# Performance work log

Hardware: AMD Instinct MI355X
Metric: run time of the kernel (lower is better)

The kernel has to match this reference:

```python
import jax, jax.numpy as jnp
import numpy as np

NUM_EXPERTS = 8
D_IN = 4096
D_OUT = 4096


def setup_inputs() -> dict:
    key = jax.random.key(0)
    k_x, k_gw, k_gb, k_ew, k_eb = jax.random.split(key, 5)
    x = jax.random.normal(k_x, (4, 2048, D_IN), dtype=jnp.float32)
    gate_w = jax.random.normal(k_gw, (NUM_EXPERTS, D_IN), dtype=jnp.float32) * 0.02
    gate_b = jax.random.normal(k_gb, (NUM_EXPERTS,), dtype=jnp.float32) * 0.02
    expert_w = jax.random.normal(k_ew, (NUM_EXPERTS, D_OUT, D_IN), dtype=jnp.float32) * 0.02
    expert_b = jax.random.normal(k_eb, (NUM_EXPERTS, D_OUT), dtype=jnp.float32) * 0.02
    return {"x": x, "gate_w": gate_w, "gate_b": gate_b,
            "expert_w": expert_w, "expert_b": expert_b}


def reference(x, gate_w, gate_b, expert_w, expert_b):
    # Flatten tokens: [T, D_IN]
    orig_shape = x.shape
    xf = x.reshape(-1, x.shape[-1])
    # Gating: softmax over logits, then top-1 (argmax of softmax == argmax of logits)
    gate_logits = xf @ gate_w.T + gate_b            # [T, E]
    gates = jax.nn.softmax(gate_logits, axis=-1)
    selected = jnp.argmax(gates, axis=-1)           # [T] int
    # Per-expert Linear applied to the tokens routed to it (dense-masked grouped GEMM).
    # Faithful to the module: top-1 dispatch, no gate-probability weighting of output.
    out = jnp.zeros((xf.shape[0], expert_w.shape[1]), dtype=xf.dtype)
    for j in range(expert_w.shape[0]):  # fixed small expert count
        yj = xf @ expert_w[j].T + expert_b[j]       # [T, D_OUT]
        out = out + jnp.where((selected == j)[:, None], yj, 0.0)
    return out.reshape(*orig_shape[:-1], expert_w.shape[1])
```

## Files before the change

### kernel.cpp

```cpp
#include <hip/hip_runtime.h>

#define NE   8
#define DIN  4096
#define DOUT 4096
#define TOK  8192

#define BM 128
#define BN 128
#define BKF 64

#define BK 32
#define LDSK 40

typedef __attribute__((ext_vector_type(4))) float f32x4;
typedef __attribute__((ext_vector_type(8))) short bf16x8;
typedef __attribute__((ext_vector_type(2))) unsigned long long u64x2;

#define AS1 __attribute__((address_space(1)))
#define AS3 __attribute__((address_space(3)))

static __device__ __forceinline__ unsigned short f2bf(float f) {
  unsigned u = __builtin_bit_cast(unsigned, f);
  u += 0x7fffu + ((u >> 16) & 1u);
  return (unsigned short)(u >> 16);
}

static __device__ __forceinline__ unsigned long long pack4(f32x4 v) {
  return (unsigned long long)f2bf(v[0])
       | ((unsigned long long)f2bf(v[1]) << 16)
       | ((unsigned long long)f2bf(v[2]) << 32)
       | ((unsigned long long)f2bf(v[3]) << 48);
}

static __device__ __forceinline__ void gload16(const void* g, void* l) {
  __builtin_amdgcn_global_load_lds((const AS1 unsigned int*)g,
                                   (AS3 unsigned int*)l, 16, 0, 0);
}

__global__ void gate_convert(const float* __restrict__ x, const float* __restrict__ gw,
                             const float* __restrict__ gb, int* __restrict__ counts,
                             int* __restrict__ tlist, unsigned short* __restrict__ xbf) {
  const int lane = threadIdx.x & 63;
  const int tok  = blockIdx.x * 4 + (threadIdx.x >> 6);
  const float* xr = x + (size_t)tok * DIN;
  unsigned short* xo = xbf + (size_t)tok * DIN;
  float acc[NE];
  #pragma unroll
  for (int e = 0; e < NE; ++e) acc[e] = 0.f;
  for (int i = lane * 4; i < DIN; i += 256) {
    f32x4 xv = *(const f32x4*)(xr + i);
    *(unsigned long long*)(xo + i) = pack4(xv);
    #pragma unroll
    for (int e = 0; e < NE; ++e) {
      f32x4 wv = *(const f32x4*)(gw + e * DIN + i);
      acc[e] += xv[0]*wv[0] + xv[1]*wv[1] + xv[2]*wv[2] + xv[3]*wv[3];
    }
  }
  #pragma unroll
  for (int e = 0; e < NE; ++e) {
    float v = acc[e];
    #pragma unroll
    for (int o = 32; o > 0; o >>= 1) v += __shfl_xor(v, o);
    acc[e] = v;
  }
  if (lane == 0) {
    float bv = acc[0] + gb[0];
    int best = 0;
    #pragma unroll
    for (int e = 1; e < NE; ++e) {
      float v = acc[e] + gb[e];
      if (v > bv) { bv = v; best = e; }
    }
    int pos = atomicAdd(&counts[best], 1);
    tlist[best * TOK + pos] = tok;
  }
}

__global__ void convw(const float* __restrict__ w, unsigned short* __restrict__ wbf) {
  const size_t n = (size_t)NE * DOUT * DIN;
  size_t idx = ((size_t)blockIdx.x * 256 + threadIdx.x) * 8;
  const size_t stride = (size_t)gridDim.x * 256 * 8;
  for (; idx < n; idx += stride) {
    f32x4 a = *(const f32x4*)(w + idx);
    f32x4 b = *(const f32x4*)(w + idx + 4);
    u64x2 v; v[0] = pack4(a); v[1] = pack4(b);
    *(u64x2*)(wbf + idx) = v;
  }
}

__global__ __launch_bounds__(256, 2)
void moe_gemm_bf(const unsigned short* __restrict__ xbf,
                 const unsigned short* __restrict__ wbf,
                 const float* __restrict__ eb,
                 const int* __restrict__ counts,
                 const int* __restrict__ tlist,
                 float* __restrict__ out) {
  __shared__ unsigned short sA[BM * BKF];
  __shared__ unsigned short sB[BN * BKF];
  __shared__ int rowtok[BM];

  const int tid  = threadIdx.x;
  const int slot = blockIdx.y;

  int e = -1, mtile = 0, Me = 0;
  {
    int acc = 0;
    #pragma unroll
    for (int j = 0; j < NE; ++j) {
      int c = counts[j];
      int t = (c + BM - 1) / BM;
      if (e < 0 && slot < acc + t) { e = j; mtile = slot - acc; Me = c; }
      acc += t;
    }
  }
  if (e < 0) return;

  const int n0 = blockIdx.x * BN;
  const int m0 = mtile * BM;

  if (tid < BM) {
    int r = m0 + tid;
    rowtok[tid] = tlist[e * TOK + (r < Me ? r : Me - 1)];
  }
  __syncthreads();

  const int lane = tid & 63;
  const int w    = tid >> 6;
  const int j8   = lane & 7;
  const int rsub = lane >> 3;
  const int colsw = ((j8 ^ rsub) * 8);

  const unsigned short* ag[4];
  const unsigned short* bg[4];
  const unsigned short* wbase = wbf + (size_t)e * DOUT * DIN;
  #pragma unroll
  for (int c = 0; c < 4; ++c) {
    int row = (w * 4 + c) * 8 + rsub;
    ag[c] = xbf   + (size_t)rowtok[row] * DIN + colsw;
    bg[c] = wbase + (size_t)(n0 + row)  * DIN + colsw;
  }

  const int wr = (w >> 1) * 64;
  const int wc = (w & 1) * 64;
  const int lr = lane & 15;
  const int lk = lane >> 4;
  const int lr7 = lr & 7;

  f32x4 acc[4][4];
  #pragma unroll
  for (int m = 0; m < 4; ++m)
    #pragma unroll
    for (int n = 0; n < 4; ++n) acc[m][n] = (f32x4){0.f, 0.f, 0.f, 0.f};

  for (int kt = 0; kt < DIN / BKF; ++kt) {
    const int kofs = kt * BKF;
    #pragma unroll
    for (int c = 0; c < 4; ++c) {
      gload16(ag[c] + kofs, &sA[(w * 4 + c) * 512]);
      gload16(bg[c] + kofs, &sB[(w * 4 + c) * 512]);
    }
    __syncthreads();

    #pragma unroll
    for (int ks = 0; ks < 2; ++ks) {
      bf16x8 af[4], bfv[4];
      #pragma unroll
      for (int m = 0; m < 4; ++m)
        af[m] = *(const bf16x8*)&sA[(wr + m * 16 + lr) * BKF + (((ks * 4 + lk) ^ lr7) * 8)];
      #pragma unroll
      for (int n = 0; n < 4; ++n)
        bfv[n] = *(const bf16x8*)&sB[(wc + n * 16 + lr) * BKF + (((ks * 4 + lk) ^ lr7) * 8)];
      #pragma unroll
      for (int m = 0; m < 4; ++m)
        #pragma unroll
        for (int n = 0; n < 4; ++n)
          acc[m][n] = __builtin_amdgcn_mfma_f32_16x16x32_bf16(af[m], bfv[n], acc[m][n], 0, 0, 0);
    }
    __syncthreads();
  }

  float bias[4];
  #pragma unroll
  for (int n = 0; n < 4; ++n) bias[n] = eb[e * DOUT + n0 + wc + n * 16 + lr];

  #pragma unroll
  for (int m = 0; m < 4; ++m) {
    #pragma unroll
    for (int j = 0; j < 4; ++j) {
      int rloc = wr + m * 16 + lk * 4 + j;
      if (m0 + rloc < Me) {
        int tokr = rowtok[rloc];
        float* op = out + (size_t)tokr * DOUT + n0 + wc;
        #pragma unroll
        for (int n = 0; n < 4; ++n)
          op[n * 16 + lr] = acc[m][n][j] + bias[n];
      }
    }
  }
}

__global__ void gate_kernel(const float* __restrict__ x, const float* __restrict__ gw,
                            const float* __restrict__ gb, int* __restrict__ counts,
                            int* __restrict__ tlist) {
  const int lane = threadIdx.x & 63;
  const int tok  = blockIdx.x * 4 + (threadIdx.x >> 6);
  const float* xr = x + (size_t)tok * DIN;
  float acc[NE];
  #pragma unroll
  for (int e = 0; e < NE; ++e) acc[e] = 0.f;
  for (int i = lane; i < DIN; i += 64) {
    float xv = xr[i];
    #pragma unroll
    for (int e = 0; e < NE; ++e) acc[e] += xv * gw[e * DIN + i];
  }
  #pragma unroll
  for (int e = 0; e < NE; ++e) {
    float v = acc[e];
    #pragma unroll
    for (int o = 32; o > 0; o >>= 1) v += __shfl_xor(v, o);
    acc[e] = v;
  }
  if (lane == 0) {
    float bv = acc[0] + gb[0];
    int best = 0;
    #pragma unroll
    for (int e = 1; e < NE; ++e) {
      float v = acc[e] + gb[e];
      if (v > bv) { bv = v; best = e; }
    }
    int pos = atomicAdd(&counts[best], 1);
    tlist[best * TOK + pos] = tok;
  }
}

__global__ __launch_bounds__(256, 2)
void moe_gemm(const float* __restrict__ x, const float* __restrict__ ew,
              const float* __restrict__ eb, const int* __restrict__ counts,
              const int* __restrict__ tlist, float* __restrict__ out) {
  __shared__ unsigned short sA[2][BM * LDSK];
  __shared__ unsigned short sB[2][BN * LDSK];
  __shared__ int rowtok[BM];

  const int tid  = threadIdx.x;
  const int slot = blockIdx.y;

  int e = -1, mtile = 0, Me = 0;
  {
    int acc = 0;
    #pragma unroll
    for (int j = 0; j < NE; ++j) {
      int c = counts[j];
      int t = (c + BM - 1) / BM;
      if (e < 0 && slot < acc + t) { e = j; mtile = slot - acc; Me = c; }
      acc += t;
    }
  }
  if (e < 0) return;

  const int n0 = blockIdx.x * BN;
  const int m0 = mtile * BM;
  const float* we = ew + (size_t)e * DOUT * DIN;

  if (tid < BM) {
    int r = m0 + tid;
    int rr = r < Me ? r : (Me - 1);
    rowtok[tid] = tlist[e * TOK + rr];
  }
  __syncthreads();

  const int srow = tid >> 3;
  const int scol = (tid & 7) * 4;
  const int lane = tid & 63;
  const int w  = tid >> 6;
  const int wr = (w >> 1) * 64;
  const int wc = (w & 1) * 64;
  const int lr = lane & 15;
  const int lk = lane >> 4;

  f32x4 accf[4][4];
  #pragma unroll
  for (int m = 0; m < 4; ++m)
    #pragma unroll
    for (int n = 0; n < 4; ++n) accf[m][n] = (f32x4){0.f, 0.f, 0.f, 0.f};

  const float* aptr[4];
  const float* bptr[4];
  #pragma unroll
  for (int p = 0; p < 4; ++p) {
    int r = p * 32 + srow;
    aptr[p] = x  + (size_t)rowtok[r] * DIN + scol;
    bptr[p] = we + (size_t)(n0 + r)  * DIN + scol;
  }

  const int NK = DIN / BK;

  #pragma unroll
  for (int p = 0; p < 4; ++p) {
    int r = p * 32 + srow;
    *(unsigned long long*)&sA[0][r * LDSK + scol] = pack4(*(const f32x4*)(aptr[p]));
    *(unsigned long long*)&sB[0][r * LDSK + scol] = pack4(*(const f32x4*)(bptr[p]));
  }
  __syncthreads();

  int cur = 0;
  for (int kt = 0; kt < NK; ++kt) {
    f32x4 ra[4], rb[4];
    const bool more = (kt + 1 < NK);
    if (more) {
      const int koff = (kt + 1) * BK;
      #pragma unroll
      for (int p = 0; p < 4; ++p) {
        ra[p] = *(const f32x4*)(aptr[p] + koff);
        rb[p] = *(const f32x4*)(bptr[p] + koff);
      }
    }
    bf16x8 af[4], bfr[4];
    #pragma unroll
    for (int m = 0; m < 4; ++m)
      af[m] = *(const bf16x8*)&sA[cur][(wr + m * 16 + lr) * LDSK + lk * 8];
    #pragma unroll
    for (int n = 0; n < 4; ++n)
      bfr[n] = *(const bf16x8*)&sB[cur][(wc + n * 16 + lr) * LDSK + lk * 8];
    #pragma unroll
    for (int m = 0; m < 4; ++m)
      #pragma unroll
      for (int n = 0; n < 4; ++n)
        accf[m][n] = __builtin_amdgcn_mfma_f32_16x16x32_bf16(af[m], bfr[n], accf[m][n], 0, 0, 0);
    if (more) {
      #pragma unroll
      for (int p = 0; p < 4; ++p) {
        int r = p * 32 + srow;
        *(unsigned long long*)&sA[cur ^ 1][r * LDSK + scol] = pack4(ra[p]);
        *(unsigned long long*)&sB[cur ^ 1][r * LDSK + scol] = pack4(rb[p]);
      }
    }
    __syncthreads();
    cur ^= 1;
  }

  float bias[4];
  #pragma unroll
  for (int n = 0; n < 4; ++n) bias[n] = eb[e * DOUT + n0 + wc + n * 16 + lr];

  #pragma unroll
  for (int m = 0; m < 4; ++m) {
    #pragma unroll
    for (int j = 0; j < 4; ++j) {
      int rloc = wr + m * 16 + lk * 4 + j;
      if (m0 + rloc < Me) {
        int tokr = rowtok[rloc];
        float* op = out + (size_t)tokr * DOUT + n0 + wc;
        #pragma unroll
        for (int n = 0; n < 4; ++n)
          op[n * 16 + lr] = accf[m][n][j] + bias[n];
      }
    }
  }
}

extern "C" void kernel_launch(void* const* d_in, const int* in_sizes, int n_in,
                              void* d_out, int out_size, void* d_ws, size_t ws_size,
                              hipStream_t stream) {
  const float* x  = (const float*)d_in[0];
  const float* gw = (const float*)d_in[1];
  const float* gb = (const float*)d_in[2];
  const float* ew = (const float*)d_in[3];
  const float* eb = (const float*)d_in[4];
  float* out = (float*)d_out;

  int* counts = (int*)d_ws;
  int* tlist  = counts + 16;
  const size_t XOFF = 1u << 20;
  const size_t WOFF = XOFF + (size_t)TOK * DIN * 2;
  const size_t NEED = WOFF + (size_t)NE * DOUT * DIN * 2;

  hipMemsetAsync(counts, 0, 16 * sizeof(int), stream);

  if (ws_size >= NEED) {
    unsigned short* xbf = (unsigned short*)((char*)d_ws + XOFF);
    unsigned short* wbf = (unsigned short*)((char*)d_ws + WOFF);
    gate_convert<<<TOK / 4, 256, 0, stream>>>(x, gw, gb, counts, tlist, xbf);
    convw<<<8192, 256, 0, stream>>>(ew, wbf);
    dim3 grid(DOUT / BN, TOK / BM + NE, 1);
    moe_gemm_bf<<<grid, 256, 0, stream>>>(xbf, wbf, eb, counts, tlist, out);
  } else {
    gate_kernel<<<TOK / 4, 256, 0, stream>>>(x, gw, gb, counts, tlist);
    dim3 grid(DOUT / BN, TOK / BM + NE, 1);
    moe_gemm<<<grid, 256, 0, stream>>>(x, ew, eb, counts, tlist, out);
  }
}
```

Before: 606.5 us.

## Use 256x256 tiles, 512 threads, triple-buffered LDS pipeline and XCD-aware block remap

Rewrites the bf16 grouped GEMM to use 256x256 output tiles with 8 waves, each wave holding a 128x64 accumulator slice. LDS becomes a 3-stage ring of BK=32 tiles filled by direct global-to-LDS loads, with vmcnt-based waits and one barrier per step instead of two. The launch becomes a 1D grid whose block IDs are remapped so consecutive tiles share an XCD, and s_setprio is raised around MFMA bursts. The larger tiles give more reuse per byte loaded but raise register pressure and can waste work on partially filled expert tiles.

```diff
diff --git a/kernel.cpp b/kernel.cpp
--- a/kernel.cpp
+++ b/kernel.cpp
@@ -5,11 +5,14 @@
 #define DOUT 4096
 #define TOK  8192
 
-#define BM 128
-#define BN 128
-#define BKF 64
-
+#define BM 256
+#define BN 256
 #define BK 32
+#define NT (DIN / BK)
+#define TSZ (BM * BK)
+
+#define FBM 128
+#define FBK 32
 #define LDSK 40
 
 typedef __attribute__((ext_vector_type(4))) float f32x4;
@@ -30,11 +33,6 @@
        | ((unsigned long long)f2bf(v[1]) << 16)
        | ((unsigned long long)f2bf(v[2]) << 32)
        | ((unsigned long long)f2bf(v[3]) << 48);
-}
-
-static __device__ __forceinline__ void gload16(const void* g, void* l) {
-  __builtin_amdgcn_global_load_lds((const AS1 unsigned int*)g,
-                                   (AS3 unsigned int*)l, 16, 0, 0);
 }
 
 __global__ void gate_convert(const float* __restrict__ x, const float* __restrict__ gw,
@@ -88,19 +86,23 @@
   }
 }
 
-__global__ __launch_bounds__(256, 2)
+__global__ __launch_bounds__(512, 2)
 void moe_gemm_bf(const unsigned short* __restrict__ xbf,
                  const unsigned short* __restrict__ wbf,
                  const float* __restrict__ eb,
                  const int* __restrict__ counts,
                  const int* __restrict__ tlist,
                  float* __restrict__ out) {
-  __shared__ unsigned short sA[BM * BKF];
-  __shared__ unsigned short sB[BN * BKF];
+  __shared__ unsigned short sA[3 * TSZ];
+  __shared__ unsigned short sB[3 * TSZ];
   __shared__ int rowtok[BM];
 
-  const int tid  = threadIdx.x;
-  const int slot = blockIdx.y;
+  const int tid = threadIdx.x;
+
+  const int cpx  = gridDim.x >> 3;
+  const int wgid = (blockIdx.x & 7) * cpx + (blockIdx.x >> 3);
+  const int ntile = wgid & 15;
+  const int slot  = wgid >> 4;
 
   int e = -1, mtile = 0, Me = 0;
   {
@@ -115,8 +117,9 @@
   }
   if (e < 0) return;
 
-  const int n0 = blockIdx.x * BN;
+  const int n0 = ntile * BN;
   const int m0 = mtile * BM;
+  const unsigned short* wbase = wbf + (size_t)e * DOUT * DIN;
 
   if (tid < BM) {
     int r = m0 + tid;
@@ -124,79 +127,117 @@
   }
   __syncthreads();
 
-  const int lane = tid & 63;
-  const int w    = tid >> 6;
-  const int j8   = lane & 7;
-  const int rsub = lane >> 3;
-  const int colsw = ((j8 ^ rsub) * 8);
-
-  const unsigned short* ag[4];
-  const unsigned short* bg[4];
-  const unsigned short* wbase = wbf + (size_t)e * DOUT * DIN;
-  #pragma unroll
-  for (int c = 0; c < 4; ++c) {
-    int row = (w * 4 + c) * 8 + rsub;
-    ag[c] = xbf   + (size_t)rowtok[row] * DIN + colsw;
-    bg[c] = wbase + (size_t)(n0 + row)  * DIN + colsw;
-  }
-
-  const int wr = (w >> 1) * 64;
-  const int wc = (w & 1) * 64;
-  const int lr = lane & 15;
-  const int lk = lane >> 4;
-  const int lr7 = lr & 7;
-
-  f32x4 acc[4][4];
-  #pragma unroll
-  for (int m = 0; m < 4; ++m)
+  const int w = tid >> 6;
+  const int l = tid & 63;
+
+  const int sr0 = w * 32 + (l >> 2);
+  const int sr1 = sr0 + 16;
+  const int c0 = ((l & 3) ^ ((sr0 >> 1) & 3)) * 8;
+  const int c1 = ((l & 3) ^ ((sr1 >> 1) & 3)) * 8;
+  const unsigned short* ga0 = xbf   + (size_t)rowtok[sr0] * DIN + c0;
+  const unsigned short* ga1 = xbf   + (size_t)rowtok[sr1] * DIN + c1;
+  const unsigned short* gb0 = wbase + (size_t)(n0 + sr0)  * DIN + c0;
+  const unsigned short* gb1 = wbase + (size_t)(n0 + sr1)  * DIN + c1;
+  const int la0 = (w * 32) * BK;
+  const int la1 = (w * 32 + 16) * BK;
+
+  const int wm = w >> 2, wn = w & 3;
+  const int lr = l & 15, lk = l >> 4;
+  int offA[8], offB[4];
+  #pragma unroll
+  for (int m = 0; m < 8; ++m) {
+    int r = wm * 128 + m * 16 + lr;
+    offA[m] = r * BK + ((lk ^ ((r >> 1) & 3)) * 8);
+  }
+  #pragma unroll
+  for (int n = 0; n < 4; ++n) {
+    int r = wn * 64 + n * 16 + lr;
+    offB[n] = r * BK + ((lk ^ ((r >> 1) & 3)) * 8);
+  }
+
+  f32x4 acc[8][4];
+  #pragma unroll
+  for (int m = 0; m < 8; ++m)
     #pragma unroll
     for (int n = 0; n < 4; ++n) acc[m][n] = (f32x4){0.f, 0.f, 0.f, 0.f};
 
-  for (int kt = 0; kt < DIN / BKF; ++kt) {
-    const int kofs = kt * BKF;
-    #pragma unroll
-    for (int c = 0; c < 4; ++c) {
-      gload16(ag[c] + kofs, &sA[(w * 4 + c) * 512]);
-      gload16(bg[c] + kofs, &sB[(w * 4 + c) * 512]);
-    }
-    __syncthreads();
-
-    #pragma unroll
-    for (int ks = 0; ks < 2; ++ks) {
-      bf16x8 af[4], bfv[4];
-      #pragma unroll
-      for (int m = 0; m < 4; ++m)
-        af[m] = *(const bf16x8*)&sA[(wr + m * 16 + lr) * BKF + (((ks * 4 + lk) ^ lr7) * 8)];
-      #pragma unroll
-      for (int n = 0; n < 4; ++n)
-        bfv[n] = *(const bf16x8*)&sB[(wc + n * 16 + lr) * BKF + (((ks * 4 + lk) ^ lr7) * 8)];
-      #pragma unroll
-      for (int m = 0; m < 4; ++m)
-        #pragma unroll
-        for (int n = 0; n < 4; ++n)
-          acc[m][n] = __builtin_amdgcn_mfma_f32_16x16x32_bf16(af[m], bfv[n], acc[m][n], 0, 0, 0);
-    }
-    __syncthreads();
-  }
+#define STAGE(kt, b) do {                                                                   \
+    const int ko_ = (kt) * BK;                                                              \
+    const int bo_ = (b) * TSZ;                                                              \
+    __builtin_amdgcn_global_load_lds((const AS1 unsigned int*)(ga0 + ko_),                  \
+                                     (AS3 unsigned int*)&sA[bo_ + la0], 16, 0, 0);          \
+    __builtin_amdgcn_global_load_lds((const AS1 unsigned int*)(ga1 + ko_),                  \
+                                     (AS3 unsigned int*)&sA[bo_ + la1], 16, 0, 0);          \
+    __builtin_amdgcn_global_load_lds((const AS1 unsigned int*)(gb0 + ko_),                  \
+                                     (AS3 unsigned int*)&sB[bo_ + la0], 16, 0, 0);          \
+    __builtin_amdgcn_global_load_lds((const AS1 unsigned int*)(gb1 + ko_),                  \
+                                     (AS3 unsigned int*)&sB[bo_ + la1], 16, 0, 0);          \
+  } while (0)
+
+#define COMPUTE(b) do {                                                                     \
+    const int bo_ = (b) * TSZ;                                                              \
+    bf16x8 bv[4], av[4];                                                                    \
+    _Pragma("unroll") for (int n = 0; n < 4; ++n)                                           \
+      bv[n] = *(const bf16x8*)&sB[bo_ + offB[n]];                                           \
+    _Pragma("unroll") for (int m = 0; m < 4; ++m)                                           \
+      av[m] = *(const bf16x8*)&sA[bo_ + offA[m]];                                           \
+    __builtin_amdgcn_s_setprio(1);                                                          \
+    _Pragma("unroll") for (int m = 0; m < 4; ++m)                                           \
+      _Pragma("unroll") for (int n = 0; n < 4; ++n)                                         \
+        acc[m][n] = __builtin_amdgcn_mfma_f32_16x16x32_bf16(av[m], bv[n], acc[m][n], 0,0,0);\
+    __builtin_amdgcn_s_setprio(0);                                                          \
+    _Pragma("unroll") for (int m = 0; m < 4; ++m)                                           \
+      av[m] = *(const bf16x8*)&sA[bo_ + offA[m + 4]];                                       \
+    __builtin_amdgcn_s_setprio(1);                                                          \
+    _Pragma("unroll") for (int m = 0; m < 4; ++m)                                           \
+      _Pragma("unroll") for (int n = 0; n < 4; ++n)                                         \
+        acc[m+4][n] = __builtin_amdgcn_mfma_f32_16x16x32_bf16(av[m], bv[n], acc[m+4][n], 0,0,0);\
+    __builtin_amdgcn_s_setprio(0);                                                          \
+  } while (0)
+
+  STAGE(0, 0);
+  STAGE(1, 1);
+  asm volatile("s_waitcnt vmcnt(4)" ::: "memory");
+  __builtin_amdgcn_s_barrier();
+  asm volatile("" ::: "memory");
+
+  int ct = 0;
+  for (int t = 0; t < NT - 2; ++t) {
+    int bn = ct + 2; if (bn >= 3) bn -= 3;
+    STAGE(t + 2, bn);
+    COMPUTE(ct);
+    asm volatile("s_waitcnt vmcnt(4)" ::: "memory");
+    __builtin_amdgcn_s_barrier();
+    asm volatile("" ::: "memory");
+    ct = (ct == 2) ? 0 : ct + 1;
+  }
+  COMPUTE(ct);
+  asm volatile("s_waitcnt vmcnt(0)" ::: "memory");
+  __builtin_amdgcn_s_barrier();
+  asm volatile("" ::: "memory");
+  ct = (ct == 2) ? 0 : ct + 1;
+  COMPUTE(ct);
 
   float bias[4];
   #pragma unroll
-  for (int n = 0; n < 4; ++n) bias[n] = eb[e * DOUT + n0 + wc + n * 16 + lr];
-
-  #pragma unroll
-  for (int m = 0; m < 4; ++m) {
+  for (int n = 0; n < 4; ++n) bias[n] = eb[e * DOUT + n0 + wn * 64 + n * 16 + lr];
+
+  #pragma unroll
+  for (int m = 0; m < 8; ++m) {
     #pragma unroll
     for (int j = 0; j < 4; ++j) {
-      int rloc = wr + m * 16 + lk * 4 + j;
+      int rloc = wm * 128 + m * 16 + lk * 4 + j;
       if (m0 + rloc < Me) {
         int tokr = rowtok[rloc];
-        float* op = out + (size_t)tokr * DOUT + n0 + wc;
+        float* op = out + (size_t)tokr * DOUT + n0 + wn * 64;
         #pragma unroll
         for (int n = 0; n < 4; ++n)
           op[n * 16 + lr] = acc[m][n][j] + bias[n];
       }
     }
   }
+#undef STAGE
+#undef COMPUTE
 }
 
 __global__ void gate_kernel(const float* __restrict__ x, const float* __restrict__ gw,
@@ -237,9 +278,9 @@
 void moe_gemm(const float* __restrict__ x, const float* __restrict__ ew,
               const float* __restrict__ eb, const int* __restrict__ counts,
               const int* __restrict__ tlist, float* __restrict__ out) {
-  __shared__ unsigned short sA[2][BM * LDSK];
-  __shared__ unsigned short sB[2][BN * LDSK];
-  __shared__ int rowtok[BM];
+  __shared__ unsigned short fA[2][FBM * LDSK];
+  __shared__ unsigned short fB[2][FBM * LDSK];
+  __shared__ int rowtok[FBM];
 
   const int tid  = threadIdx.x;
   const int slot = blockIdx.y;
@@ -250,21 +291,20 @@
     #pragma unroll
     for (int j = 0; j < NE; ++j) {
       int c = counts[j];
-      int t = (c + BM - 1) / BM;
+      int t = (c + FBM - 1) / FBM;
       if (e < 0 && slot < acc + t) { e = j; mtile = slot - acc; Me = c; }
       acc += t;
     }
   }
   if (e < 0) return;
 
-  const int n0 = blockIdx.x * BN;
-  const int m0 = mtile * BM;
+  const int n0 = blockIdx.x * FBM;
+  const int m0 = mtile * FBM;
   const float* we = ew + (size_t)e * DOUT * DIN;
 
-  if (tid < BM) {
+  if (tid < FBM) {
     int r = m0 + tid;
-    int rr = r < Me ? r : (Me - 1);
-    rowtok[tid] = tlist[e * TOK + rr];
+    rowtok[tid] = tlist[e * TOK + (r < Me ? r : Me - 1)];
   }
   __syncthreads();
 
@@ -292,22 +332,20 @@
     bptr[p] = we + (size_t)(n0 + r)  * DIN + scol;
   }
 
-  const int NK = DIN / BK;
-
   #pragma unroll
   for (int p = 0; p < 4; ++p) {
     int r = p * 32 + srow;
-    *(unsigned long long*)&sA[0][r * LDSK + scol] = pack4(*(const f32x4*)(aptr[p]));
-    *(unsigned long long*)&sB[0][r * LDSK + scol] = pack4(*(const f32x4*)(bptr[p]));
+    *(unsigned long long*)&fA[0][r * LDSK + scol] = pack4(*(const f32x4*)(aptr[p]));
+    *(unsigned long long*)&fB[0][r * LDSK + scol] = pack4(*(const f32x4*)(bptr[p]));
   }
   __syncthreads();
 
   int cur = 0;
-  for (int kt = 0; kt < NK; ++kt) {
+  for (int kt = 0; kt < DIN / FBK; ++kt) {
     f32x4 ra[4], rb[4];
-    const bool more = (kt + 1 < NK);
+    const bool more = (kt + 1 < DIN / FBK);
     if (more) {
-      const int koff = (kt + 1) * BK;
+      const int koff = (kt + 1) * FBK;
       #pragma unroll
       for (int p = 0; p < 4; ++p) {
         ra[p] = *(const f32x4*)(aptr[p] + koff);
@@ -317,10 +355,10 @@
     bf16x8 af[4], bfr[4];
     #pragma unroll
     for (int m = 0; m < 4; ++m)
-      af[m] = *(const bf16x8*)&sA[cur][(wr + m * 16 + lr) * LDSK + lk * 8];
+      af[m] = *(const bf16x8*)&fA[cur][(wr + m * 16 + lr) * LDSK + lk * 8];
     #pragma unroll
     for (int n = 0; n < 4; ++n)
-      bfr[n] = *(const bf16x8*)&sB[cur][(wc + n * 16 + lr) * LDSK + lk * 8];
+      bfr[n] = *(const bf16x8*)&fB[cur][(wc + n * 16 + lr) * LDSK + lk * 8];
     #pragma unroll
     for (int m = 0; m < 4; ++m)
       #pragma unroll
@@ -330,8 +368,8 @@
       #pragma unroll
       for (int p = 0; p < 4; ++p) {
         int r = p * 32 + srow;
-        *(unsigned long long*)&sA[cur ^ 1][r * LDSK + scol] = pack4(ra[p]);
-        *(unsigned long long*)&sB[cur ^ 1][r * LDSK + scol] = pack4(rb[p]);
+        *(unsigned long long*)&fA[cur ^ 1][r * LDSK + scol] = pack4(ra[p]);
+        *(unsigned long long*)&fB[cur ^ 1][r * LDSK + scol] = pack4(rb[p]);
       }
     }
     __syncthreads();
@@ -381,11 +419,10 @@
     unsigned short* wbf = (unsigned short*)((char*)d_ws + WOFF);
     gate_convert<<<TOK / 4, 256, 0, stream>>>(x, gw, gb, counts, tlist, xbf);
     convw<<<8192, 256, 0, stream>>>(ew, wbf);
-    dim3 grid(DOUT / BN, TOK / BM + NE, 1);
-    moe_gemm_bf<<<grid, 256, 0, stream>>>(xbf, wbf, eb, counts, tlist, out);
+    moe_gemm_bf<<<16 * (TOK / BM + NE), 512, 0, stream>>>(xbf, wbf, eb, counts, tlist, out);
   } else {
     gate_kernel<<<TOK / 4, 256, 0, stream>>>(x, gw, gb, counts, tlist);
-    dim3 grid(DOUT / BN, TOK / BM + NE, 1);
+    dim3 grid(DOUT / FBM, TOK / FBM + NE, 1);
     moe_gemm<<<grid, 256, 0, stream>>>(x, ew, eb, counts, tlist, out);
   }
 }
```

Measured after the change: 835.7 us. 37.8% more time.
